# Optimization experiments

Hardware: AMD Instinct MI355X
Metric: run time of the kernel (lower is better)

The kernel has to match this reference:

```python
import jax, jax.numpy as jnp
import numpy as np

H = W = 2048
TANH_C = 1.1486328125  # probability-correction constant from the model
DEG2RAD = np.float32(np.pi / 180.0)

# Fire-spread direction angle (degrees, East=0, counterclockwise) from the
# neighbor at 3x3 window position (r, c) toward the center cell.
DIR_DEG = jnp.array([[315., 270., 225.],
                     [  0.,   0., 180.],
                     [ 45.,  90., 135.]], dtype=jnp.float32)
CENTER_MASK = jnp.ones((3, 3), jnp.float32).at[1, 1].set(0.0)  # exclude self


def _neighborhood(x):
    """x: [H,W] -> [H,W,3,3] with [i,j,r,c] = x[i+r-1, j+c-1], zero padded."""
    xp = jnp.pad(x, 1)
    return jnp.stack(
        [jnp.stack([xp[r:r + H, c:c + W] for c in range(3)], axis=-1)
         for r in range(3)], axis=-2)


def setup_inputs() -> dict:
    key = jax.random.key(0)
    ks = jax.random.split(key, 8)
    p_veg = jax.random.uniform(ks[0], (H, W), jnp.float32)
    p_den = jax.random.uniform(ks[1], (H, W), jnp.float32)
    wind_velocity = jax.random.uniform(ks[2], (H, W), jnp.float32) * 10.0
    wind_towards_direction = jax.random.uniform(ks[3], (H, W), jnp.float32) * 360.0
    slope = (jax.random.uniform(ks[4], (H, W, 3, 3), jnp.float32) - 0.5) * 60.0
    burning = jax.random.uniform(ks[5], (H, W)) < 0.01  # sparse initial ignition
    burned = jnp.zeros((H, W), dtype=bool)
    rand_ignite = jax.random.uniform(ks[6], (H, W), jnp.float32)
    rand_continue = jax.random.uniform(ks[7], (H, W), jnp.float32)
    return dict(
        p_veg=p_veg, p_den=p_den,
        wind_velocity=wind_velocity, wind_towards_direction=wind_towards_direction,
        slope=slope,
        a=jnp.float32(0.1), p_h=jnp.float32(0.3),
        c_1=jnp.float32(0.1), c_2=jnp.float32(0.1), p_continue=jnp.float32(0.3),
        rand_ignite=rand_ignite, rand_continue=rand_continue,
        burning=burning, burned=burned,
    )


def reference(p_veg, p_den, wind_velocity, wind_towards_direction, slope,
              a, p_h, c_1, c_2, p_continue,
              rand_ignite, rand_continue, burning, burned):
    # p_w = exp(c1*V) * exp(c2*V*(cos(theta_w)-1)), theta_w = angle between
    # wind direction and per-neighbor spread direction. [H,W,3,3]
    theta_w = (wind_towards_direction[..., None, None] - DIR_DEG) * DEG2RAD
    p_w = (jnp.exp(c_1 * wind_velocity)[..., None, None]
           * jnp.exp(c_2 * wind_velocity[..., None, None] * (jnp.cos(theta_w) - 1.0)))
    # p_s = exp(a * theta_s), slope angle in radians. [H,W,3,3]
    p_s = jnp.exp(a * slope * DEG2RAD)
    # p_propagate = tanh(c * p_h*(1+p_veg)*(1+p_den)*p_w*p_s)
    p_base = p_h * (1.0 + p_veg) * (1.0 + p_den)  # [H,W]
    p_prop = jnp.tanh(TANH_C * (p_base[..., None, None] * p_w * p_s))
    # 8-neighbor burning indicators (center masked out). [H,W,3,3]
    nbr_burning = _neighborhood(burning.astype(jnp.float32)) * CENTER_MASK
    # p_ignite = 1 - prod_j (1 - p_propagate_j * burning_j)
    p_ignite = 1.0 - jnp.prod(1.0 - p_prop * nbr_burning, axis=(-2, -1))
    # Stochastic state transition.
    burnable = ~burning & ~burned
    new_ignited = burnable & (rand_ignite < p_ignite)
    keep = burning & (rand_continue < p_continue)
    new_burning = new_ignited | keep
    new_burned = burned | (burning & ~keep)
    return p_ignite, jnp.stack([new_burning, new_burned])
```

## Files before the change

### kernel.cpp

```cpp
#include <hip/hip_runtime.h>
#include <math.h>

namespace {

constexpr int H = 2048;
constexpr int W = 2048;
constexpr float TANH_C  = 1.1486328125f;
constexpr float DEG2RAD = 0.017453292519943295f;
constexpr float RT2H    = 0.70710678118654752f;
constexpr float BAND    = 2.5e-4f;

__global__ __launch_bounds__(256) void wildfire_step(
    const float* __restrict__ p_veg,  const float* __restrict__ p_den,
    const float* __restrict__ wind_v, const float* __restrict__ wind_d,
    const float* __restrict__ slope,
    const float* __restrict__ s_a,  const float* __restrict__ s_ph,
    const float* __restrict__ s_c1, const float* __restrict__ s_c2,
    const float* __restrict__ s_pc,
    const float* __restrict__ rand_ig, const float* __restrict__ rand_co,
    const int* __restrict__ burning, const int* __restrict__ burned,
    float* __restrict__ out)
{
    __shared__ float sb[3][260];
    __shared__ __align__(16) float ssl[256 * 9];
    const int t  = (int)threadIdx.x;
    const int i  = (int)blockIdx.y;
    const int j0 = (int)blockIdx.x * 256;
    const int j  = j0 + t;
    const int idx = i * W + j;

    {
        const float4* sg  = reinterpret_cast<const float4*>(slope + (size_t)(i * W + j0) * 9);
        float4*       sl4 = reinterpret_cast<float4*>(ssl);
        sl4[t]       = sg[t];
        sl4[256 + t] = sg[256 + t];
        if (t < 64) sl4[512 + t] = sg[512 + t];
    }

    for (int r = 0; r < 3; ++r) {
        const int ii = i + r - 1;
        for (int c = t; c < 258; c += 256) {
            const int jj = j0 - 1 + c;
            float v = 0.f;
            if (ii >= 0 && ii < H && jj >= 0 && jj < W)
                v = burning[ii * W + jj] ? 1.f : 0.f;
            sb[r][c] = v;
        }
    }

    const float pv  = p_veg[idx];
    const float pd  = p_den[idx];
    const float wv  = wind_v[idx];
    const float wd  = wind_d[idx];
    const float rig = rand_ig[idx];
    const float rco = rand_co[idx];
    const int   wb  = burned[idx];

    const float a      = s_a[0];
    const float p_h    = s_ph[0];
    const float c1     = s_c1[0];
    const float c2     = s_c2[0];
    const float p_cont = s_pc[0];

    __syncthreads();

    const float b0 = sb[0][t], b1 = sb[0][t+1], b2 = sb[0][t+2];
    const float b3 = sb[1][t], bc = sb[1][t+1], b5 = sb[1][t+2];
    const float b6 = sb[2][t], b7 = sb[2][t+1], b8 = sb[2][t+2];

    const bool  is_burning = (bc != 0.f);
    const float any_n = b0 + b1 + b2 + b3 + b5 + b6 + b7 + b8;

    const float* sl = ssl + t * 9;

    float p_ignite    = 0.f;
    bool  new_ignited = false;

    if (__any(any_n != 0.f)) {
        const float wr  = wd * DEG2RAD;
        const float cw  = __cosf(wr);
        const float sw  = __sinf(wr);
        const float ew  = __expf(c1 * wv);
        const float cvw = c2 * wv;
        const float asl = a * DEG2RAD;
        const float p_base = (p_h * (1.f + pv)) * (1.f + pd);
        const float Cz2 = 2.f * (TANH_C * (p_base * ew));

#define NB(K, b, CK, SK, si)                                                \
        const float ct##K = fmaf(cw, (CK), sw * (SK));                      \
        const float eu##K = __expf(fmaf(cvw, ct##K - 1.f, asl * sl[si]));   \
        const float E##K  = __expf(Cz2 * eu##K);                            \
        const float d##K  = fmaf((b), E##K, 1.f);

        NB(0, b0,  RT2H, -RT2H, 0)
        NB(1, b1,  0.f,  -1.f,  1)
        NB(2, b2, -RT2H, -RT2H, 2)
        NB(3, b3,  1.f,   0.f,  3)
        NB(5, b5, -1.f,   0.f,  5)
        NB(6, b6,  RT2H,  RT2H, 6)
        NB(7, b7,  0.f,   1.f,  7)
        NB(8, b8, -RT2H,  RT2H, 8)
#undef NB
        const float den = ((d0 * d1) * (d2 * d3)) * ((d5 * d6) * (d7 * d8));
        const float num = (float)(1 << (int)any_n);
        p_ignite = 1.f - num * __builtin_amdgcn_rcpf(den);

        new_ignited = (!is_burning) && (wb == 0) && (rig < p_ignite);

        const bool need = (any_n != 0.f) && (fabsf(rig - p_ignite) < BAND);
        if (__any((int)need)) {
            if (need) {
                const float ewp = expf(c1 * wv);
                float prod = 1.f;
#define NBP(b, dirdeg, si)                                                  \
                if ((b) != 0.f) {                                           \
                    const float th = (wd - (dirdeg)) * DEG2RAD;             \
                    const float pw = ewp * expf(cvw * (cosf(th) - 1.f));    \
                    const float ps = expf((a * sl[si]) * DEG2RAD);          \
                    const float pp = tanhf(TANH_C * ((p_base * pw) * ps));  \
                    prod *= 1.f - pp * (b);                                 \
                }
                NBP(b0, 315.f, 0)
                NBP(b1, 270.f, 1)
                NBP(b2, 225.f, 2)
                NBP(b3,   0.f, 3)
                NBP(b5, 180.f, 5)
                NBP(b6,  45.f, 6)
                NBP(b7,  90.f, 7)
                NBP(b8, 135.f, 8)
#undef NBP
                p_ignite    = 1.f - prod;
                new_ignited = (!is_burning) && (wb == 0) && (rig < p_ignite);
            }
        }
    }

    const bool keep = is_burning && (rco < p_cont);
    const bool nb   = new_ignited || keep;
    const bool nd   = (wb != 0) || (is_burning && !keep);

    out[idx]             = p_ignite;
    out[H * W + idx]     = nb ? 1.f : 0.f;
    out[2 * H * W + idx] = nd ? 1.f : 0.f;
}

}

extern "C" void kernel_launch(void* const* d_in, const int* in_sizes, int n_in,
                              void* d_out, int out_size, void* d_ws, size_t ws_size,
                              hipStream_t stream)
{
    (void)in_sizes; (void)n_in; (void)out_size; (void)d_ws; (void)ws_size;
    dim3 grid(W / 256, H, 1);
    dim3 block(256, 1, 1);
    hipLaunchKernelGGL(wildfire_step, grid, block, 0, stream,
        (const float*)d_in[0],  (const float*)d_in[1],
        (const float*)d_in[2],  (const float*)d_in[3],
        (const float*)d_in[4],
        (const float*)d_in[5],  (const float*)d_in[6],
        (const float*)d_in[7],  (const float*)d_in[8],
        (const float*)d_in[9],
        (const float*)d_in[10], (const float*)d_in[11],
        (const int*)d_in[12],   (const int*)d_in[13],
        (float*)d_out);
}
```

Before: 331.9 us.

## Process four cells per thread with vectorized float4 loads and stores

Each thread now handles four consecutive columns, loading all per-cell inputs, the slope stencil and burning rows as float4/int4 vectors and writing the three outputs as float4. The slope is read straight into registers instead of staged through shared memory, and the shared burning halo is widened to 1024 columns plus edge cells. This cuts load/store instruction count and grid size for a memory-bound kernel, at the cost of more registers per thread and fewer blocks (2048*2), which may lower occupancy and latency hiding.

```diff
diff --git a/kernel.cpp b/kernel.cpp
--- a/kernel.cpp
+++ b/kernel.cpp
@@ -5,6 +5,7 @@
 
 constexpr int H = 2048;
 constexpr int W = 2048;
+constexpr int CPT = 4;
 constexpr float TANH_C  = 1.1486328125f;
 constexpr float DEG2RAD = 0.017453292519943295f;
 constexpr float RT2H    = 0.70710678118654752f;
@@ -21,127 +22,150 @@
     const int* __restrict__ burning, const int* __restrict__ burned,
     float* __restrict__ out)
 {
-    __shared__ float sb[3][260];
-    __shared__ __align__(16) float ssl[256 * 9];
-    const int t  = (int)threadIdx.x;
-    const int i  = (int)blockIdx.y;
-    const int j0 = (int)blockIdx.x * 256;
-    const int j  = j0 + t;
-    const int idx = i * W + j;
+    __shared__ float sb[3][1032];
+    const int t    = (int)threadIdx.x;
+    const int i    = (int)blockIdx.y;
+    const int j0   = (int)blockIdx.x * (256 * CPT);
+    const int idx0 = i * W + j0 + CPT * t;
 
+    const float4 pv4  = *(const float4*)(p_veg  + idx0);
+    const float4 pd4  = *(const float4*)(p_den  + idx0);
+    const float4 wv4  = *(const float4*)(wind_v + idx0);
+    const float4 wd4  = *(const float4*)(wind_d + idx0);
+    const float4 rig4 = *(const float4*)(rand_ig + idx0);
+    const float4 rco4 = *(const float4*)(rand_co + idx0);
+    const int4   bd4  = *(const int4*)  (burned + idx0);
+
+    float4 sl4[9];
     {
-        const float4* sg  = reinterpret_cast<const float4*>(slope + (size_t)(i * W + j0) * 9);
-        float4*       sl4 = reinterpret_cast<float4*>(ssl);
-        sl4[t]       = sg[t];
-        sl4[256 + t] = sg[256 + t];
-        if (t < 64) sl4[512 + t] = sg[512 + t];
+        const float4* sg = (const float4*)(slope + (size_t)idx0 * 9);
+        #pragma unroll
+        for (int k = 0; k < 9; ++k) sl4[k] = sg[k];
     }
+    const float* sl = (const float*)sl4;
 
+    #pragma unroll
     for (int r = 0; r < 3; ++r) {
-        const int ii = i + r - 1;
-        for (int c = t; c < 258; c += 256) {
-            const int jj = j0 - 1 + c;
-            float v = 0.f;
-            if (ii >= 0 && ii < H && jj >= 0 && jj < W)
-                v = burning[ii * W + jj] ? 1.f : 0.f;
-            sb[r][c] = v;
-        }
+        const int ii = i - 1 + r;
+        int4 b4 = make_int4(0, 0, 0, 0);
+        if (ii >= 0 && ii < H)
+            b4 = *(const int4*)(burning + (size_t)ii * W + j0 + CPT * t);
+        float4 f;
+        f.x = b4.x ? 1.f : 0.f; f.y = b4.y ? 1.f : 0.f;
+        f.z = b4.z ? 1.f : 0.f; f.w = b4.w ? 1.f : 0.f;
+        *(float4*)&sb[r][4 + CPT * t] = f;
     }
-
-    const float pv  = p_veg[idx];
-    const float pd  = p_den[idx];
-    const float wv  = wind_v[idx];
-    const float wd  = wind_d[idx];
-    const float rig = rand_ig[idx];
-    const float rco = rand_co[idx];
-    const int   wb  = burned[idx];
+    if (t < 6) {
+        const int r  = t >> 1, side = t & 1;
+        const int ii = i - 1 + r;
+        const int jj = side ? (j0 + 1024) : (j0 - 1);
+        float v = 0.f;
+        if (ii >= 0 && ii < H && jj >= 0 && jj < W)
+            v = burning[(size_t)ii * W + jj] ? 1.f : 0.f;
+        sb[r][side ? 1028 : 3] = v;
+    }
 
     const float a      = s_a[0];
     const float p_h    = s_ph[0];
     const float c1     = s_c1[0];
     const float c2     = s_c2[0];
     const float p_cont = s_pc[0];
+    const float asl    = a * DEG2RAD;
 
     __syncthreads();
 
-    const float b0 = sb[0][t], b1 = sb[0][t+1], b2 = sb[0][t+2];
-    const float b3 = sb[1][t], bc = sb[1][t+1], b5 = sb[1][t+2];
-    const float b6 = sb[2][t], b7 = sb[2][t+1], b8 = sb[2][t+2];
+    const float pvv[4] = {pv4.x, pv4.y, pv4.z, pv4.w};
+    const float pdv[4] = {pd4.x, pd4.y, pd4.z, pd4.w};
+    const float wvv[4] = {wv4.x, wv4.y, wv4.z, wv4.w};
+    const float wdv[4] = {wd4.x, wd4.y, wd4.z, wd4.w};
+    const float rgv[4] = {rig4.x, rig4.y, rig4.z, rig4.w};
+    const float rcv[4] = {rco4.x, rco4.y, rco4.z, rco4.w};
+    const int   bdv[4] = {bd4.x, bd4.y, bd4.z, bd4.w};
 
-    const bool  is_burning = (bc != 0.f);
-    const float any_n = b0 + b1 + b2 + b3 + b5 + b6 + b7 + b8;
+    float pig[4], nbo[4], ndo[4];
 
-    const float* sl = ssl + t * 9;
+    #pragma unroll
+    for (int u = 0; u < CPT; ++u) {
+        const int c = 4 + CPT * t + u;
+        const float b0 = sb[0][c-1], b1 = sb[0][c], b2 = sb[0][c+1];
+        const float b3 = sb[1][c-1], bc = sb[1][c], b5 = sb[1][c+1];
+        const float b6 = sb[2][c-1], b7 = sb[2][c], b8 = sb[2][c+1];
 
-    float p_ignite    = 0.f;
-    bool  new_ignited = false;
+        const bool  is_burning = (bc != 0.f);
+        const float any_n = b0 + b1 + b2 + b3 + b5 + b6 + b7 + b8;
 
-    if (__any(any_n != 0.f)) {
-        const float wr  = wd * DEG2RAD;
-        const float cw  = __cosf(wr);
-        const float sw  = __sinf(wr);
-        const float ew  = __expf(c1 * wv);
-        const float cvw = c2 * wv;
-        const float asl = a * DEG2RAD;
-        const float p_base = (p_h * (1.f + pv)) * (1.f + pd);
-        const float Cz2 = 2.f * (TANH_C * (p_base * ew));
+        float p_ig   = 0.f;
+        bool  new_ig = false;
 
-#define NB(K, b, CK, SK, si)                                                \
-        const float ct##K = fmaf(cw, (CK), sw * (SK));                      \
-        const float eu##K = __expf(fmaf(cvw, ct##K - 1.f, asl * sl[si]));   \
-        const float E##K  = __expf(Cz2 * eu##K);                            \
-        const float d##K  = fmaf((b), E##K, 1.f);
+        if (__any(any_n != 0.f)) {
+            const float wd  = wdv[u];
+            const float wv  = wvv[u];
+            const float wr  = wd * DEG2RAD;
+            const float cw  = __cosf(wr);
+            const float sw  = __sinf(wr);
+            const float ew  = __expf(c1 * wv);
+            const float cvw = c2 * wv;
+            const float p_base = (p_h * (1.f + pvv[u])) * (1.f + pdv[u]);
+            const float Cz2 = 2.f * (TANH_C * (p_base * ew));
 
-        NB(0, b0,  RT2H, -RT2H, 0)
-        NB(1, b1,  0.f,  -1.f,  1)
-        NB(2, b2, -RT2H, -RT2H, 2)
-        NB(3, b3,  1.f,   0.f,  3)
-        NB(5, b5, -1.f,   0.f,  5)
-        NB(6, b6,  RT2H,  RT2H, 6)
-        NB(7, b7,  0.f,   1.f,  7)
-        NB(8, b8, -RT2H,  RT2H, 8)
+#define NB(K, b, CK, SK, si)                                                   \
+            const float ct##K = fmaf(cw, (CK), sw * (SK));                     \
+            const float eu##K = __expf(fmaf(cvw, ct##K - 1.f, asl * sl[9*u + si])); \
+            const float E##K  = __expf(Cz2 * eu##K);                           \
+            const float d##K  = fmaf((b), E##K, 1.f);
+
+            NB(0, b0,  RT2H, -RT2H, 0)
+            NB(1, b1,  0.f,  -1.f,  1)
+            NB(2, b2, -RT2H, -RT2H, 2)
+            NB(3, b3,  1.f,   0.f,  3)
+            NB(5, b5, -1.f,   0.f,  5)
+            NB(6, b6,  RT2H,  RT2H, 6)
+            NB(7, b7,  0.f,   1.f,  7)
+            NB(8, b8, -RT2H,  RT2H, 8)
 #undef NB
-        const float den = ((d0 * d1) * (d2 * d3)) * ((d5 * d6) * (d7 * d8));
-        const float num = (float)(1 << (int)any_n);
-        p_ignite = 1.f - num * __builtin_amdgcn_rcpf(den);
+            const float den = ((d0 * d1) * (d2 * d3)) * ((d5 * d6) * (d7 * d8));
+            const float num = (float)(1 << (int)any_n);
+            p_ig = 1.f - num * __builtin_amdgcn_rcpf(den);
 
-        new_ignited = (!is_burning) && (wb == 0) && (rig < p_ignite);
+            new_ig = (!is_burning) && (bdv[u] == 0) && (rgv[u] < p_ig);
 
-        const bool need = (any_n != 0.f) && (fabsf(rig - p_ignite) < BAND);
-        if (__any((int)need)) {
-            if (need) {
-                const float ewp = expf(c1 * wv);
-                float prod = 1.f;
-#define NBP(b, dirdeg, si)                                                  \
-                if ((b) != 0.f) {                                           \
-                    const float th = (wd - (dirdeg)) * DEG2RAD;             \
-                    const float pw = ewp * expf(cvw * (cosf(th) - 1.f));    \
-                    const float ps = expf((a * sl[si]) * DEG2RAD);          \
-                    const float pp = tanhf(TANH_C * ((p_base * pw) * ps));  \
-                    prod *= 1.f - pp * (b);                                 \
+            const bool need = (any_n != 0.f) && (fabsf(rgv[u] - p_ig) < BAND);
+            if (__any((int)need)) {
+                if (need) {
+                    const float ewp = expf(c1 * wv);
+                    float prod = 1.f;
+#define NBP(b, dirdeg, si)                                                     \
+                    if ((b) != 0.f) {                                          \
+                        const float th = (wd - (dirdeg)) * DEG2RAD;            \
+                        const float pw = ewp * expf(cvw * (cosf(th) - 1.f));   \
+                        const float ps = expf((a * sl[9*u + si]) * DEG2RAD);   \
+                        const float pp = tanhf(TANH_C * ((p_base * pw) * ps)); \
+                        prod *= 1.f - pp * (b);                                \
+                    }
+                    NBP(b0, 315.f, 0)
+                    NBP(b1, 270.f, 1)
+                    NBP(b2, 225.f, 2)
+                    NBP(b3,   0.f, 3)
+                    NBP(b5, 180.f, 5)
+                    NBP(b6,  45.f, 6)
+                    NBP(b7,  90.f, 7)
+                    NBP(b8, 135.f, 8)
+#undef NBP
+                    p_ig   = 1.f - prod;
+                    new_ig = (!is_burning) && (bdv[u] == 0) && (rgv[u] < p_ig);
                 }
-                NBP(b0, 315.f, 0)
-                NBP(b1, 270.f, 1)
-                NBP(b2, 225.f, 2)
-                NBP(b3,   0.f, 3)
-                NBP(b5, 180.f, 5)
-                NBP(b6,  45.f, 6)
-                NBP(b7,  90.f, 7)
-                NBP(b8, 135.f, 8)
-#undef NBP
-                p_ignite    = 1.f - prod;
-                new_ignited = (!is_burning) && (wb == 0) && (rig < p_ignite);
             }
         }
+
+        const bool keep = is_burning && (rcv[u] < p_cont);
+        pig[u] = p_ig;
+        nbo[u] = (new_ig || keep) ? 1.f : 0.f;
+        ndo[u] = ((bdv[u] != 0) || (is_burning && !keep)) ? 1.f : 0.f;
     }
 
-    const bool keep = is_burning && (rco < p_cont);
-    const bool nb   = new_ignited || keep;
-    const bool nd   = (wb != 0) || (is_burning && !keep);
-
-    out[idx]             = p_ignite;
-    out[H * W + idx]     = nb ? 1.f : 0.f;
-    out[2 * H * W + idx] = nd ? 1.f : 0.f;
+    *(float4*)(out + idx0)             = make_float4(pig[0], pig[1], pig[2], pig[3]);
+    *(float4*)(out + H * W + idx0)     = make_float4(nbo[0], nbo[1], nbo[2], nbo[3]);
+    *(float4*)(out + 2 * H * W + idx0) = make_float4(ndo[0], ndo[1], ndo[2], ndo[3]);
 }
 
 }
@@ -151,7 +175,7 @@
                               hipStream_t stream)
 {
     (void)in_sizes; (void)n_in; (void)out_size; (void)d_ws; (void)ws_size;
-    dim3 grid(W / 256, H, 1);
+    dim3 grid(W / (256 * CPT), H, 1);
     dim3 block(256, 1, 1);
     hipLaunchKernelGGL(wildfire_step, grid, block, 0, stream,
         (const float*)d_in[0],  (const float*)d_in[1],
```

Result: no change. 336.6 us (+1.4%).
